# Kernel optimization log

Hardware: AMD Instinct MI355X
Metric: run time of the kernel (lower is better)

## Reference

```python
import jax, jax.numpy as jnp
import numpy as np


def setup_inputs() -> dict:
    key = jax.random.key(0)
    ks = jax.random.split(key, 11)
    d = 64
    inp = {
        "query_emb": jax.random.normal(ks[0], (d,), dtype=jnp.float32),
        "prog_embs": jax.random.normal(ks[1], (262144, d), dtype=jnp.float32),
        "stack_embs": jax.random.normal(ks[2], (131072, d), dtype=jnp.float32),
        "local_embs": jax.random.normal(ks[3], (131072, d), dtype=jnp.float32),
        "heap_embs": jax.random.normal(ks[4], (262144, d), dtype=jnp.float32),
        "call_embs": jax.random.normal(ks[5], (32768, d), dtype=jnp.float32),
        "WQ": jax.random.normal(ks[6], (10, 2, d), dtype=jnp.float32),
        "bQ": jax.random.normal(ks[7], (10, 2), dtype=jnp.float32),
        "WK": jax.random.normal(ks[8], (10, 2, d), dtype=jnp.float32),
        "WV1": jax.random.normal(ks[9], (9, 1, d), dtype=jnp.float32),
        "WV_call": jax.random.normal(ks[10], (1, 3, d), dtype=jnp.float32),
    }
    return inp


def _lookup(query_emb, mem, wq, bq, wk, wv):
    """Hard-max attention for a group of heads sharing one memory bank.
    wq/wk: [h,2,d], bq: [h,2], wv: [h,v,d], mem: [n,d]."""
    q = jnp.einsum('htd,d->ht', wq, query_emb) + bq          # [h,2]
    scores = jnp.einsum('htd,nd,ht->hn', wk, mem, q)         # K @ q per head
    best = jnp.argmax(scores, axis=1)                        # [h]
    best_scores = jnp.take_along_axis(scores, best[:, None], axis=1)[:, 0]
    vals = jnp.einsum('hvd,hd->hv', wv, mem[best])           # V[best] per head
    return vals, best_scores, best


def reference(query_emb, prog_embs, stack_embs, local_embs, heap_embs,
              call_embs, WQ, bQ, WK, WV1, WV_call):
    # head routing: 0-1 prog, 2-4 stack, 5-6 local, 7-8 heap, 9 call(v_dim=3)
    v_p, s_p, b_p = _lookup(query_emb, prog_embs,  WQ[0:2], bQ[0:2], WK[0:2], WV1[0:2])
    v_s, s_s, b_s = _lookup(query_emb, stack_embs, WQ[2:5], bQ[2:5], WK[2:5], WV1[2:5])
    v_l, s_l, b_l = _lookup(query_emb, local_embs, WQ[5:7], bQ[5:7], WK[5:7], WV1[5:7])
    v_h, s_h, b_h = _lookup(query_emb, heap_embs,  WQ[7:9], bQ[7:9], WK[7:9], WV1[7:9])
    v_c, s_c, b_c = _lookup(query_emb, call_embs,  WQ[9:10], bQ[9:10], WK[9:10], WV_call)
    values = jnp.concatenate([v_p.ravel(), v_s.ravel(), v_l.ravel(),
                              v_h.ravel(), v_c.ravel()])       # [12]
    best_scores = jnp.concatenate([s_p, s_s, s_l, s_h, s_c])   # [10]
    best_idx = jnp.concatenate([b_p, b_s, b_l, b_h, b_c])      # [10]
    return values, best_scores, best_idx
```

## Files before the change

### kernel.cpp

```cpp
#include <hip/hip_runtime.h>
#include <math.h>

__device__ __constant__ int HOFF[10] = {0, 512, 1024, 1280, 1536, 1792, 2048, 2304, 2816, 3328};
__device__ __constant__ int HCNT[10] = {512, 512, 256, 256, 256, 256, 256, 512, 512, 64};

static __device__ __forceinline__ unsigned int fkey(float f) {
  unsigned int u = __float_as_uint(f);
  return (u & 0x80000000u) ? ~u : (u | 0x80000000u);
}
static __device__ __forceinline__ float funkey(unsigned int k) {
  unsigned int u = (k & 0x80000000u) ? (k & 0x7fffffffu) : ~k;
  return __uint_as_float(u);
}
static __device__ __forceinline__ float dot4(float4 a, float4 b) {
  return a.x * b.x + a.y * b.y + a.z * b.z + a.w * b.w;
}

__global__ __launch_bounds__(256) void scan_kernel(
    const float* __restrict__ query,
    const float* __restrict__ prog, const float* __restrict__ stck,
    const float* __restrict__ locl, const float* __restrict__ heap,
    const float* __restrict__ call,
    const float* __restrict__ WQ, const float* __restrict__ bQ,
    const float* __restrict__ WK, float* __restrict__ ws)
{
  unsigned long long* res = (unsigned long long*)ws;
  int b = blockIdx.x, tid = threadIdx.x;

  const float* mem; int h0, nh, brank, off0, off1, off2;
  if (b < 512)       { mem = prog; h0 = 0; nh = 2; brank = b;        off0 = 0    + brank; off1 = 512  + brank; off2 = 0; }
  else if (b < 768)  { mem = stck; h0 = 2; nh = 3; brank = b - 512;  off0 = 1024 + brank; off1 = 1280 + brank; off2 = 1536 + brank; }
  else if (b < 1024) { mem = locl; h0 = 5; nh = 2; brank = b - 768;  off0 = 1792 + brank; off1 = 2048 + brank; off2 = 0; }
  else if (b < 1536) { mem = heap; h0 = 7; nh = 2; brank = b - 1024; off0 = 2304 + brank; off1 = 2816 + brank; off2 = 0; }
  else               { mem = call; h0 = 9; nh = 1; brank = b - 1536; off0 = 3328 + brank; off1 = 0;            off2 = 0; }

  __shared__ float qs[6];
  __shared__ float skeff[3][64];
  if (tid < 2 * nh) {
    int t = tid;
    const float* wq = WQ + (h0 * 2 + t) * 64;
    float s = bQ[h0 * 2 + t];
    for (int d = 0; d < 64; ++d) s += wq[d] * query[d];
    qs[t] = s;
  }
  __syncthreads();
  if (tid < 192) {
    int i = tid >> 6, d = tid & 63;
    float v = 0.f;
    if (i < nh) {
      int h = h0 + i;
      v = qs[2 * i] * WK[(h * 2) * 64 + d] + qs[2 * i + 1] * WK[(h * 2 + 1) * 64 + d];
    }
    skeff[i][d] = v;
  }
  __syncthreads();

  int lane4 = tid & 3, rsub = tid >> 2;

  float4 ka[4], kb[4], kc[4];
#pragma unroll
  for (int j = 0; j < 4; ++j) {
    ka[j] = ((const float4*)skeff[0])[j * 4 + lane4];
    kb[j] = ((const float4*)skeff[1])[j * 4 + lane4];
    kc[j] = ((const float4*)skeff[2])[j * 4 + lane4];
  }

  float bsA = -INFINITY, bsB = -INFINITY, bsC = -INFINITY;
  int biA = 0, biB = 0, biC = 0;
  int base = brank * 512;
#pragma unroll 2
  for (int it = 0; it < 8; ++it) {
    int r = base + it * 64 + rsub;
    const float* rowp = mem + (size_t)r * 64 + lane4 * 4;
    float4 v0 = *(const float4*)(rowp +  0);
    float4 v1 = *(const float4*)(rowp + 16);
    float4 v2 = *(const float4*)(rowp + 32);
    float4 v3 = *(const float4*)(rowp + 48);

    float sA = dot4(v0, ka[0]) + dot4(v1, ka[1]) + dot4(v2, ka[2]) + dot4(v3, ka[3]);
    float sB = dot4(v0, kb[0]) + dot4(v1, kb[1]) + dot4(v2, kb[2]) + dot4(v3, kb[3]);
    float sC = dot4(v0, kc[0]) + dot4(v1, kc[1]) + dot4(v2, kc[2]) + dot4(v3, kc[3]);

    sA += __shfl_xor(sA, 1); sA += __shfl_xor(sA, 2);
    sB += __shfl_xor(sB, 1); sB += __shfl_xor(sB, 2);
    sC += __shfl_xor(sC, 1); sC += __shfl_xor(sC, 2);

    if (sA > bsA) { bsA = sA; biA = r; }
    if (sB > bsB) { bsB = sB; biB = r; }
    if (sC > bsC) { bsC = sC; biC = r; }
  }

  unsigned long long p0 = ((unsigned long long)fkey(bsA) << 32) | (unsigned long long)(0xFFFFFFFFu - (unsigned)biA);
  unsigned long long p1 = ((unsigned long long)fkey(bsB) << 32) | (unsigned long long)(0xFFFFFFFFu - (unsigned)biB);
  unsigned long long p2 = ((unsigned long long)fkey(bsC) << 32) | (unsigned long long)(0xFFFFFFFFu - (unsigned)biC);
#pragma unroll
  for (int m = 4; m < 64; m <<= 1) {
    unsigned long long t;
    t = __shfl_xor(p0, m); if (t > p0) p0 = t;
    t = __shfl_xor(p1, m); if (t > p1) p1 = t;
    t = __shfl_xor(p2, m); if (t > p2) p2 = t;
  }
  __shared__ unsigned long long red[3][4];
  int wv = tid >> 6;
  if ((tid & 63) == 0) { red[0][wv] = p0; red[1][wv] = p1; red[2][wv] = p2; }
  __syncthreads();
  if (tid == 0) {
    unsigned long long m0 = red[0][0], m1 = red[1][0], m2 = red[2][0];
#pragma unroll
    for (int w = 1; w < 4; ++w) {
      if (red[0][w] > m0) m0 = red[0][w];
      if (red[1][w] > m1) m1 = red[1][w];
      if (red[2][w] > m2) m2 = red[2][w];
    }
    res[off0] = m0;
    if (nh > 1) res[off1] = m1;
    if (nh > 2) res[off2] = m2;
  }
}

__global__ __launch_bounds__(640) void epi_kernel(
    const float* __restrict__ prog, const float* __restrict__ stck,
    const float* __restrict__ locl, const float* __restrict__ heap,
    const float* __restrict__ call,
    const float* __restrict__ WV1, const float* __restrict__ WVc,
    const float* __restrict__ ws, float* __restrict__ out) {
  const unsigned long long* res = (const unsigned long long*)ws;
  __shared__ int sidx[10];
  int tid = threadIdx.x;
  int w = tid >> 6, lane = tid & 63;
  if (w < 10) {
    const unsigned long long* basep = res + HOFF[w];
    int n = HCNT[w];
    unsigned long long m = 0ull;
    for (int i = lane; i < n; i += 64) {
      unsigned long long v = basep[i];
      if (v > m) m = v;
    }
#pragma unroll
    for (int s = 1; s < 64; s <<= 1) {
      unsigned long long t = __shfl_xor(m, s);
      if (t > m) m = t;
    }
    if (lane == 0) {
      unsigned int key = (unsigned int)(m >> 32);
      int idx = (int)(0xFFFFFFFFu - (unsigned int)(m & 0xFFFFFFFFull));
      sidx[w] = idx;
      out[12 + w] = funkey(key);
      out[22 + w] = (float)idx;
    }
  }
  __syncthreads();
  int p = tid >> 4, l = tid & 15;
  if (p < 12) {
    int hh = (p < 9) ? p : 9;
    const float* wrow = (p < 9) ? (WV1 + p * 64) : (WVc + (p - 9) * 64);
    const float* vmem;
    if (hh < 2) vmem = prog;
    else if (hh < 5) vmem = stck;
    else if (hh < 7) vmem = locl;
    else if (hh < 9) vmem = heap;
    else vmem = call;
    const float* row = vmem + (size_t)sidx[hh] * 64;
    float s = 0.f;
#pragma unroll
    for (int j = 0; j < 4; ++j) s += wrow[l * 4 + j] * row[l * 4 + j];
#pragma unroll
    for (int m2 = 1; m2 < 16; m2 <<= 1) s += __shfl_xor(s, m2);
    if (l == 0) out[p] = s;
  }
}

extern "C" void kernel_launch(void* const* d_in, const int* in_sizes, int n_in,
                              void* d_out, int out_size, void* d_ws, size_t ws_size,
                              hipStream_t stream) {
  const float* query = (const float*)d_in[0];
  const float* prog  = (const float*)d_in[1];
  const float* stck  = (const float*)d_in[2];
  const float* locl  = (const float*)d_in[3];
  const float* heap  = (const float*)d_in[4];
  const float* call  = (const float*)d_in[5];
  const float* WQ    = (const float*)d_in[6];
  const float* bQ    = (const float*)d_in[7];
  const float* WK    = (const float*)d_in[8];
  const float* WV1   = (const float*)d_in[9];
  const float* WVc   = (const float*)d_in[10];
  float* ws  = (float*)d_ws;
  float* out = (float*)d_out;

  hipLaunchKernelGGL(scan_kernel, dim3(1600), dim3(256), 0, stream,
                     query, prog, stck, locl, heap, call, WQ, bQ, WK, ws);
  hipLaunchKernelGGL(epi_kernel, dim3(1), dim3(640), 0, stream,
                     prog, stck, locl, heap, call, WV1, WVc, ws, out);
}
```

Before: 47.33 us.

## Switch scan to one thread per row with four rows each and halve grid

Each thread now computes full 64-wide dot products for four rows spaced 256 apart, instead of four lanes cooperating on one row. This removes the per-row xor shuffles and the running argmax inside the loop, and doubles the rows per block so the grid and the partial-result layout are halved. In exchange, each load instruction now touches addresses 256 bytes apart across adjacent threads, so accesses are far less coalesced. The kernel depends more on cache-line reuse across the unrolled loop, and it also uses more registers.

```diff
diff --git a/kernel.cpp b/kernel.cpp
--- a/kernel.cpp
+++ b/kernel.cpp
@@ -1,8 +1,8 @@
 #include <hip/hip_runtime.h>
 #include <math.h>
 
-__device__ __constant__ int HOFF[10] = {0, 512, 1024, 1280, 1536, 1792, 2048, 2304, 2816, 3328};
-__device__ __constant__ int HCNT[10] = {512, 512, 256, 256, 256, 256, 256, 512, 512, 64};
+__device__ __constant__ int HOFF[10] = {0, 256, 512, 640, 768, 896, 1024, 1152, 1408, 1664};
+__device__ __constant__ int HCNT[10] = {256, 256, 128, 128, 128, 128, 128, 256, 256, 32};
 
 static __device__ __forceinline__ unsigned int fkey(float f) {
   unsigned int u = __float_as_uint(f);
@@ -28,73 +28,72 @@
   int b = blockIdx.x, tid = threadIdx.x;
 
   const float* mem; int h0, nh, brank, off0, off1, off2;
-  if (b < 512)       { mem = prog; h0 = 0; nh = 2; brank = b;        off0 = 0    + brank; off1 = 512  + brank; off2 = 0; }
-  else if (b < 768)  { mem = stck; h0 = 2; nh = 3; brank = b - 512;  off0 = 1024 + brank; off1 = 1280 + brank; off2 = 1536 + brank; }
-  else if (b < 1024) { mem = locl; h0 = 5; nh = 2; brank = b - 768;  off0 = 1792 + brank; off1 = 2048 + brank; off2 = 0; }
-  else if (b < 1536) { mem = heap; h0 = 7; nh = 2; brank = b - 1024; off0 = 2304 + brank; off1 = 2816 + brank; off2 = 0; }
-  else               { mem = call; h0 = 9; nh = 1; brank = b - 1536; off0 = 3328 + brank; off1 = 0;            off2 = 0; }
+  if (b < 256)      { mem = prog; h0 = 0; nh = 2; brank = b;       off0 = 0    + brank; off1 = 256 + brank;  off2 = 0; }
+  else if (b < 384) { mem = stck; h0 = 2; nh = 3; brank = b - 256; off0 = 512  + brank; off1 = 640 + brank;  off2 = 768 + brank; }
+  else if (b < 512) { mem = locl; h0 = 5; nh = 2; brank = b - 384; off0 = 896  + brank; off1 = 1024 + brank; off2 = 0; }
+  else if (b < 768) { mem = heap; h0 = 7; nh = 2; brank = b - 512; off0 = 1152 + brank; off1 = 1408 + brank; off2 = 0; }
+  else              { mem = call; h0 = 9; nh = 1; brank = b - 768; off0 = 1664 + brank; off1 = 0;            off2 = 0; }
 
   __shared__ float qs[6];
   __shared__ float skeff[3][64];
   if (tid < 2 * nh) {
-    int t = tid;
-    const float* wq = WQ + (h0 * 2 + t) * 64;
-    float s = bQ[h0 * 2 + t];
+    const float* wq = WQ + (h0 * 2 + tid) * 64;
+    float s = bQ[h0 * 2 + tid];
     for (int d = 0; d < 64; ++d) s += wq[d] * query[d];
-    qs[t] = s;
+    qs[tid] = s;
   }
   __syncthreads();
   if (tid < 192) {
-    int i = tid >> 6, d = tid & 63;
+    int hi = tid >> 6, d = tid & 63;
     float v = 0.f;
-    if (i < nh) {
-      int h = h0 + i;
-      v = qs[2 * i] * WK[(h * 2) * 64 + d] + qs[2 * i + 1] * WK[(h * 2 + 1) * 64 + d];
+    if (hi < nh) {
+      int h = h0 + hi;
+      v = qs[2 * hi] * WK[(h * 2) * 64 + d] + qs[2 * hi + 1] * WK[(h * 2 + 1) * 64 + d];
     }
-    skeff[i][d] = v;
+    skeff[hi][d] = v;
   }
   __syncthreads();
 
-  int lane4 = tid & 3, rsub = tid >> 2;
+  int base = brank * 1024;
+  const float* r0 = mem + (size_t)(base + tid) * 64;
+  float a0 = 0.f, a1 = 0.f, a2 = 0.f, a3 = 0.f;
+  float b0 = 0.f, b1 = 0.f, b2 = 0.f, b3 = 0.f;
+  float c0 = 0.f, c1 = 0.f, c2 = 0.f, c3 = 0.f;
 
-  float4 ka[4], kb[4], kc[4];
 #pragma unroll
-  for (int j = 0; j < 4; ++j) {
-    ka[j] = ((const float4*)skeff[0])[j * 4 + lane4];
-    kb[j] = ((const float4*)skeff[1])[j * 4 + lane4];
-    kc[j] = ((const float4*)skeff[2])[j * 4 + lane4];
+  for (int j = 0; j < 16; ++j) {
+    float4 kA = ((const float4*)skeff[0])[j];
+    float4 kB = ((const float4*)skeff[1])[j];
+    float4 kC = ((const float4*)skeff[2])[j];
+    float4 v0 = *(const float4*)(r0 + j * 4);
+    float4 v1 = *(const float4*)(r0 + 256 * 64 + j * 4);
+    float4 v2 = *(const float4*)(r0 + 512 * 64 + j * 4);
+    float4 v3 = *(const float4*)(r0 + 768 * 64 + j * 4);
+
+    a0 += dot4(v0, kA); a1 += dot4(v1, kA); a2 += dot4(v2, kA); a3 += dot4(v3, kA);
+    b0 += dot4(v0, kB); b1 += dot4(v1, kB); b2 += dot4(v2, kB); b3 += dot4(v3, kB);
+    c0 += dot4(v0, kC); c1 += dot4(v1, kC); c2 += dot4(v2, kC); c3 += dot4(v3, kC);
   }
 
-  float bsA = -INFINITY, bsB = -INFINITY, bsC = -INFINITY;
-  int biA = 0, biB = 0, biC = 0;
-  int base = brank * 512;
-#pragma unroll 2
-  for (int it = 0; it < 8; ++it) {
-    int r = base + it * 64 + rsub;
-    const float* rowp = mem + (size_t)r * 64 + lane4 * 4;
-    float4 v0 = *(const float4*)(rowp +  0);
-    float4 v1 = *(const float4*)(rowp + 16);
-    float4 v2 = *(const float4*)(rowp + 32);
-    float4 v3 = *(const float4*)(rowp + 48);
-
-    float sA = dot4(v0, ka[0]) + dot4(v1, ka[1]) + dot4(v2, ka[2]) + dot4(v3, ka[3]);
-    float sB = dot4(v0, kb[0]) + dot4(v1, kb[1]) + dot4(v2, kb[2]) + dot4(v3, kb[3]);
-    float sC = dot4(v0, kc[0]) + dot4(v1, kc[1]) + dot4(v2, kc[2]) + dot4(v3, kc[3]);
-
-    sA += __shfl_xor(sA, 1); sA += __shfl_xor(sA, 2);
-    sB += __shfl_xor(sB, 1); sB += __shfl_xor(sB, 2);
-    sC += __shfl_xor(sC, 1); sC += __shfl_xor(sC, 2);
-
-    if (sA > bsA) { bsA = sA; biA = r; }
-    if (sB > bsB) { bsB = sB; biB = r; }
-    if (sC > bsC) { bsC = sC; biC = r; }
-  }
+  int rI = base + tid;
+  float bsA = a0; int biA = rI;
+  if (a1 > bsA) { bsA = a1; biA = rI + 256; }
+  if (a2 > bsA) { bsA = a2; biA = rI + 512; }
+  if (a3 > bsA) { bsA = a3; biA = rI + 768; }
+  float bsB = b0; int biB = rI;
+  if (b1 > bsB) { bsB = b1; biB = rI + 256; }
+  if (b2 > bsB) { bsB = b2; biB = rI + 512; }
+  if (b3 > bsB) { bsB = b3; biB = rI + 768; }
+  float bsC = c0; int biC = rI;
+  if (c1 > bsC) { bsC = c1; biC = rI + 256; }
+  if (c2 > bsC) { bsC = c2; biC = rI + 512; }
+  if (c3 > bsC) { bsC = c3; biC = rI + 768; }
 
   unsigned long long p0 = ((unsigned long long)fkey(bsA) << 32) | (unsigned long long)(0xFFFFFFFFu - (unsigned)biA);
   unsigned long long p1 = ((unsigned long long)fkey(bsB) << 32) | (unsigned long long)(0xFFFFFFFFu - (unsigned)biB);
   unsigned long long p2 = ((unsigned long long)fkey(bsC) << 32) | (unsigned long long)(0xFFFFFFFFu - (unsigned)biC);
 #pragma unroll
-  for (int m = 4; m < 64; m <<= 1) {
+  for (int m = 1; m < 64; m <<= 1) {
     unsigned long long t;
     t = __shfl_xor(p0, m); if (t > p0) p0 = t;
     t = __shfl_xor(p1, m); if (t > p1) p1 = t;
@@ -187,7 +186,7 @@
   float* ws  = (float*)d_ws;
   float* out = (float*)d_out;
 
-  hipLaunchKernelGGL(scan_kernel, dim3(1600), dim3(256), 0, stream,
+  hipLaunchKernelGGL(scan_kernel, dim3(800), dim3(256), 0, stream,
                      query, prog, stck, locl, heap, call, WQ, bQ, WK, ws);
   hipLaunchKernelGGL(epi_kernel, dim3(1), dim3(640), 0, stream,
                      prog, stck, locl, heap, call, WV1, WVc, ws, out);
```

After: 135.3 us. 2.86x slower.
